# Kernel optimization log

Measured on AMD Instinct MI355X. Metric: run time of the kernel, lower is better.

The kernel has to match this reference:

```python
import jax, jax.numpy as jnp
import numpy as np

H, HD, C = 16, 64, 64            # num_heads, head_dim, mini_batch_size
BASE_LR = 1.0
EPS = 1e-6                        # ttt LN eps (ln_fwd / ln_fused_l2_bwd)


def _l2norm(x):
    return x / jnp.maximum(jnp.linalg.norm(x, axis=-1, keepdims=True), 1e-12)


def _ln_fwd(x, g, b):
    mu = x.mean(-1, keepdims=True)
    var = x.var(-1, keepdims=True)
    return g * ((x - mu) * jax.lax.rsqrt(var + EPS)) + b


def _ln_l2_bwd(x, tgt, g, b):
    # gradient of ||LN(x)*g+b - tgt||^2 / 2 wrt x
    D = x.shape[-1]
    mu = x.mean(-1, keepdims=True)
    var = x.var(-1, keepdims=True)
    std = jnp.sqrt(var + EPS)
    xh = (x - mu) / std
    gout = (g * xh + b) - tgt
    gxh = gout * g
    return (D * gxh - gxh.sum(-1, keepdims=True) - xh * (gxh * xh).sum(-1, keepdims=True)) / (D * std)


def setup_inputs() -> dict:
    key = jax.random.key(0)
    ks = jax.random.split(key, 12)
    B, L, D = 4, 8192, 1024
    std = 0.02
    return {
        'hidden_states': jax.random.normal(ks[0], (B, L, D), jnp.float32),
        'wq_w': jax.random.normal(ks[1], (D, D), jnp.float32) * std,
        'wq_b': jnp.zeros((D,), jnp.float32),
        'wk_w': jax.random.normal(ks[2], (D, D), jnp.float32) * std,
        'wk_b': jnp.zeros((D,), jnp.float32),
        'wv_w': jax.random.normal(ks[3], (D, D), jnp.float32) * std,
        'wv_b': jnp.zeros((D,), jnp.float32),
        'wo_w': jax.random.normal(ks[4], (D, D), jnp.float32) * std,
        'wo_b': jnp.zeros((D,), jnp.float32),
        'ttt_norm_weight': jnp.ones((H, HD), jnp.float32),
        'ttt_norm_bias': jnp.zeros((H, HD), jnp.float32),
        'ttt_lr_weight': jax.random.normal(ks[5], (H, 1, D), jnp.float32) * std,
        'ttt_lr_bias': jnp.zeros((H, 1), jnp.float32),
        'W1': jax.random.normal(ks[6], (H, HD, HD), jnp.float32) * std,
        'b1': jnp.zeros((H, 1, HD), jnp.float32),
        'post_norm_w': jnp.ones((D,), jnp.float32),
        'post_norm_b': jnp.zeros((D,), jnp.float32),
    }


def _forward(hidden_states, wq_w, wq_b, wk_w, wk_b, wv_w, wv_b, wo_w, wo_b,
             ttt_norm_weight, ttt_norm_bias, ttt_lr_weight, ttt_lr_bias,
             W1, b1, post_norm_w, post_norm_b):
    B, L, D = hidden_states.shape
    NC = L // C
    XQ = (hidden_states @ wq_w.T + wq_b).reshape(B, L, H, HD)
    XK = (hidden_states @ wk_w.T + wk_b).reshape(B, L, H, HD)
    XV = (hidden_states @ wv_w.T + wv_b).reshape(B, L, H, HD)
    XQ = _l2norm(XQ)
    XK = _l2norm(XK)
    # ln_reconstruction_target (uses sample std, ddof=1, eps=1e-5 on std)
    d = XV - XK
    mu = d.mean(-1, keepdims=True)
    sd = d.std(-1, keepdims=True, ddof=1)
    XV = ttt_norm_weight[None, None] * ((d - mu) / (sd + 1e-5)) + ttt_norm_bias[None, None] + XK
    # reshape to mini-batches: [B,H,NC,C,HD]
    Xmb = hidden_states.reshape(B, NC, C, D)
    to_mb = lambda t: t.transpose(0, 2, 1, 3).reshape(B, H, NC, C, HD)
    XQ, XK, XV = to_mb(XQ), to_mb(XK), to_mb(XV)
    # eta: sigmoid lr gate per token, row-broadcast over mini-batch
    ttt_lr = jax.nn.sigmoid(jnp.einsum('bnkc,hdc->bhnkd', Xmb, ttt_lr_weight)
                            + ttt_lr_bias.reshape(1, H, 1, 1, 1))     # [B,H,NC,C,1]
    eta = jnp.swapaxes(ttt_lr, -1, -2) * (BASE_LR / HD / C)           # [B,H,NC,1,C]
    mask = jnp.tril(jnp.ones((C, C), hidden_states.dtype))
    g = ttt_norm_weight[None, :, None, :]
    bta = ttt_norm_bias[None, :, None, :]
    W0 = jnp.broadcast_to(W1[None], (B, H, HD, HD))
    b0 = jnp.broadcast_to(b1[None], (B, H, 1, HD))

    def step(carry, xs):
        W, bvec = carry
        xq, xk, xv, eta_row = xs                      # eta_row: [B,H,1,C]
        Z1 = xk @ W + bvec                            # [B,H,C,HD]
        grad = _ln_l2_bwd(Z1, xv - xk, g, bta)        # [B,H,C,HD]
        Attn = mask * jnp.einsum('bhid,bhjd->bhij', xq, xk)   # [B,H,C,C]
        eta_full = jnp.broadcast_to(eta_row, Attn.shape)      # [B,H,C,C]
        b1_bar = bvec - (mask * eta_full) @ grad              # [B,H,C,HD]
        Z1_bar = xq @ W - (eta_full * Attn) @ grad + b1_bar
        last_eta = eta_full[..., -1, :, None]                 # [B,H,C,1]
        W_new = W - jnp.einsum('bhcd,bhce->bhde', last_eta * xk, grad)
        b_new = bvec - (last_eta * grad).sum(-2, keepdims=True)
        out = xq + _ln_fwd(Z1_bar, g, bta)
        return (W_new, b_new), out

    xs = (jnp.moveaxis(XQ, 2, 0), jnp.moveaxis(XK, 2, 0),
          jnp.moveaxis(XV, 2, 0), jnp.moveaxis(eta, 2, 0))
    _, outs = jax.lax.scan(step, (W0, b0), xs)        # outs: [NC,B,H,C,HD]
    y = jnp.moveaxis(outs, 0, 2).reshape(B, H, L, HD).transpose(0, 2, 1, 3).reshape(B, L, D)
    # post LayerNorm (eps=1e-6) + output projection
    mu2 = y.mean(-1, keepdims=True)
    var2 = y.var(-1, keepdims=True)
    y = post_norm_w * ((y - mu2) * jax.lax.rsqrt(var2 + 1e-6)) + post_norm_b
    return y @ wo_w.T + wo_b


def reference(hidden_states, wq_w, wq_b, wk_w, wk_b, wv_w, wv_b, wo_w, wo_b,
              ttt_norm_weight, ttt_norm_bias, ttt_lr_weight, ttt_lr_bias,
              W1, b1, post_norm_w, post_norm_b):
    return _forward(hidden_states, wq_w, wq_b, wk_w, wk_b, wv_w, wv_b, wo_w, wo_b,
                    ttt_norm_weight, ttt_norm_bias, ttt_lr_weight, ttt_lr_bias,
                    W1, b1, post_norm_w, post_norm_b)
```

## Files before the change

kernel.cpp:

```cpp
#include <hip/hip_runtime.h>


typedef __attribute__((ext_vector_type(8))) short short8;
typedef __attribute__((ext_vector_type(4))) float f32x4;
typedef __attribute__((ext_vector_type(4))) unsigned short us4;

__device__ __forceinline__ float bf2f(unsigned short s) {
  union { unsigned int u; float f; } c;
  c.u = ((unsigned int)s) << 16;
  return c.f;
}
__device__ __forceinline__ unsigned short f2bf(float f) {
  union { float f; unsigned int u; } c;
  c.f = f;
  unsigned int u = c.u;
  return (unsigned short)((u + 0x7FFFu + ((u >> 16) & 1u)) >> 16);
}

__device__ __forceinline__ void gload_lds16(const void* g, void* l) {
  __builtin_amdgcn_global_load_lds(
      (const __attribute__((address_space(1))) unsigned int*)g,
      (__attribute__((address_space(3))) unsigned int*)l, 16, 0, 0);
}

__device__ __forceinline__ float dpp16_sum(float x) {
  int v = __float_as_int(x);
  x += __int_as_float(__builtin_amdgcn_update_dpp(v, v, 0xB1, 0xF, 0xF, true));
  v = __float_as_int(x);
  x += __int_as_float(__builtin_amdgcn_update_dpp(v, v, 0x4E, 0xF, 0xF, true));
  v = __float_as_int(x);
  x += __int_as_float(__builtin_amdgcn_update_dpp(v, v, 0x141, 0xF, 0xF, true));
  v = __float_as_int(x);
  x += __int_as_float(__builtin_amdgcn_update_dpp(v, v, 0x140, 0xF, 0xF, true));
  return x;
}

__device__ __forceinline__ void barrier_fast() {
  __builtin_amdgcn_sched_barrier(0);
  asm volatile("s_waitcnt lgkmcnt(0)" ::: "memory");
  __builtin_amdgcn_s_barrier();
  asm volatile("" ::: "memory");
  __builtin_amdgcn_sched_barrier(0);
}
__device__ __forceinline__ void bar_nowait() {
  __builtin_amdgcn_sched_barrier(0);
  asm volatile("" ::: "memory");
  __builtin_amdgcn_s_barrier();
  asm volatile("" ::: "memory");
  __builtin_amdgcn_sched_barrier(0);
}

__global__ __launch_bounds__(256) void cvt_f32_bf16(
    const float* __restrict__ in, unsigned short* __restrict__ out, long n) {
  long i = ((long)blockIdx.x * 256 + threadIdx.x) * 4;
  if (i + 3 < n) {
    float4 v = *(const float4*)&in[i];
    us4 o = { f2bf(v.x), f2bf(v.y), f2bf(v.z), f2bf(v.w) };
    *(us4*)&out[i] = o;
  }
}

__global__ __launch_bounds__(256) void build_wcat(
    const float* __restrict__ wq, const float* __restrict__ wk,
    const float* __restrict__ wv, const float* __restrict__ lrw,
    const float* __restrict__ wqb, const float* __restrict__ wkb,
    const float* __restrict__ wvb, const float* __restrict__ lrb,
    unsigned short* __restrict__ Wcat, float* __restrict__ biasc) {
  int i = blockIdx.x * 256 + threadIdx.x;
  int row = i >> 10, col = i & 1023;
  int h = row >> 8, o = row & 255;
  float v;
  if (o < 64)        v = wq[(h * 64 + o) * 1024 + col];
  else if (o < 128)  v = wk[(h * 64 + o - 64) * 1024 + col];
  else if (o < 192)  v = wv[(h * 64 + o - 128) * 1024 + col];
  else if (o == 192) v = lrw[h * 1024 + col];
  else               v = 0.f;
  Wcat[i] = f2bf(v);
  if (i < 4096) {
    int hh = i >> 8, oo = i & 255;
    float bv;
    if (oo < 64)        bv = wqb[hh * 64 + oo];
    else if (oo < 128)  bv = wkb[hh * 64 + oo - 64];
    else if (oo < 192)  bv = wvb[hh * 64 + oo - 128];
    else if (oo == 192) bv = lrb[hh];
    else                bv = 0.f;
    biasc[i] = bv;
  }
}


__global__ __launch_bounds__(512, 1) void gemm256_qkv(
    const unsigned short* __restrict__ A, const unsigned short* __restrict__ B,
    const float* __restrict__ bias, const float* __restrict__ tnw,
    const float* __restrict__ tnb, unsigned short* __restrict__ XQn,
    unsigned short* __restrict__ XKn, unsigned short* __restrict__ TGT,
    float* __restrict__ eta, long M, long K) {
  __shared__ __align__(16) unsigned short g_lds[49152];
  char* ldsc = (char*)g_lds;
  const int tid = threadIdx.x, lane = tid & 63, wid = tid >> 6;
  const int wm = wid >> 2, wn = wid & 3;
  const int l15 = lane & 15, lg = lane >> 4;
  const int NTILN = 16;

  unsigned nwg = gridDim.x, bid = blockIdx.x;
  unsigned cpx = nwg >> 3;
  unsigned swz = (bid & 7) * cpx + (bid >> 3);
  unsigned nidx = swz % (unsigned)NTILN, midx = swz / (unsigned)NTILN;
  const long m0 = (long)midx * 256, n0 = (long)nidx * 256;
  const long ldab = K * 2;

  const int srow = wid * 16 + (lane >> 2);
  const int scol = ((lane & 3) * 16) ^ (((lane >> 3) & 3) << 4);
  const int sdst = wid * 1024;
  const char* Ab = (const char*)A;
  const char* Bb = (const char*)B;

  const int acol = (lg * 16) ^ (((l15 >> 1) & 3) << 4);
  const int aro = (wm * 128 + l15) * 64 + acol;
  const int bro = 16384 + (wn * 64 + l15) * 64 + acol;

#define STG_A(tt, h, bb)                                                      \
  gload_lds16(Ab + (size_t)(m0 + (h) * 128 + srow) * ldab + (size_t)(tt) * 64 \
                  + scol,                                                     \
              ldsc + (bb) * 32768 + (h) * 8192 + sdst)
#define STG_B(tt, h, bb)                                                      \
  gload_lds16(Bb + (size_t)(n0 + (h) * 128 + srow) * ldab + (size_t)(tt) * 64 \
                  + scol,                                                     \
              ldsc + (bb) * 32768 + 16384 + (h) * 8192 + sdst)

  f32x4 acc[8][4];
#pragma unroll
  for (int m = 0; m < 8; ++m)
#pragma unroll
    for (int n = 0; n < 4; ++n) acc[m][n] = (f32x4){0.f, 0.f, 0.f, 0.f};

  const int NT = (int)(K >> 5);

  STG_A(0, 0, 0); STG_A(0, 1, 0); STG_B(0, 0, 0); STG_B(0, 1, 0);
  STG_A(1, 0, 1); STG_A(1, 1, 1); STG_B(1, 0, 1); STG_B(1, 1, 1);
  asm volatile("s_waitcnt vmcnt(4)" ::: "memory");
  bar_nowait();

  int buf = 0, sb = 2;
#pragma unroll 1
  for (int t = 0; t < NT; ++t) {
    if (t + 2 < NT) {
      STG_A(t + 2, 0, sb); STG_A(t + 2, 1, sb);
      STG_B(t + 2, 0, sb); STG_B(t + 2, 1, sb);
    }
    const char* ab = ldsc + buf * 32768 + aro;
    const char* bb2 = ldsc + buf * 32768 + bro;
    short8 av[8], bv[4];
#pragma unroll
    for (int i = 0; i < 8; ++i) av[i] = *(const short8*)(ab + i * 1024);
#pragma unroll
    for (int nf = 0; nf < 4; ++nf) bv[nf] = *(const short8*)(bb2 + nf * 1024);
    __builtin_amdgcn_s_setprio(1);
#pragma unroll
    for (int i = 0; i < 8; ++i)
#pragma unroll
      for (int nf = 0; nf < 4; ++nf)
        acc[i][nf] = __builtin_amdgcn_mfma_f32_16x16x32_bf16(av[i], bv[nf],
                                                             acc[i][nf], 0, 0, 0);
    __builtin_amdgcn_s_setprio(0);
    asm volatile("s_waitcnt vmcnt(4)" ::: "memory");
    bar_nowait();
    buf = (buf == 2) ? 0 : buf + 1;
    sb = (sb == 2) ? 0 : sb + 1;
  }
#undef STG_A
#undef STG_B

  const int h = (int)nidx;
  float bcol[4], twv[4], tbv[4];
#pragma unroll
  for (int nf = 0; nf < 4; ++nf) {
    bcol[nf] = bias[n0 + wn * 64 + nf * 16 + l15];
    twv[nf] = tnw[h * 64 + nf * 16 + l15];
    tbv[nf] = tnb[h * 64 + nf * 16 + l15];
  }
  __syncthreads();
  unsigned short* kn_s = g_lds;

  if (wn == 0) {
#pragma unroll
    for (int mf = 0; mf < 8; ++mf)
#pragma unroll
      for (int j = 0; j < 4; ++j) {
        float v[4], s2 = 0.f;
#pragma unroll
        for (int nf = 0; nf < 4; ++nf) {
          v[nf] = acc[mf][nf][j] + bcol[nf];
          s2 += v[nf] * v[nf];
        }
        s2 = dpp16_sum(s2);
        float rn = 1.f / fmaxf(sqrtf(s2), 1e-12f);
        size_t tt = (size_t)(m0 + wm * 128 + mf * 16 + lg * 4 + j);
#pragma unroll
        for (int nf = 0; nf < 4; ++nf)
          XQn[tt * 1024 + h * 64 + nf * 16 + l15] = f2bf(v[nf] * rn);
      }
  } else if (wn == 1) {
#pragma unroll
    for (int mf = 0; mf < 8; ++mf)
#pragma unroll
      for (int j = 0; j < 4; ++j) {
        float v[4], s2 = 0.f;
#pragma unroll
        for (int nf = 0; nf < 4; ++nf) {
          v[nf] = acc[mf][nf][j] + bcol[nf];
          s2 += v[nf] * v[nf];
        }
        s2 = dpp16_sum(s2);
        float rn = 1.f / fmaxf(sqrtf(s2), 1e-12f);
        size_t tt = (size_t)(m0 + wm * 128 + mf * 16 + lg * 4 + j);
        int lr_ = wm * 128 + mf * 16 + lg * 4 + j;
#pragma unroll
        for (int nf = 0; nf < 4; ++nf) {
          unsigned short kb = f2bf(v[nf] * rn);
          XKn[tt * 1024 + h * 64 + nf * 16 + l15] = kb;
          kn_s[lr_ * 72 + nf * 16 + l15] = kb;
        }
      }
  }
  __syncthreads();
  if (wn == 2) {
#pragma unroll
    for (int mf = 0; mf < 8; ++mf)
#pragma unroll
      for (int j = 0; j < 4; ++j) {
        int lr_ = wm * 128 + mf * 16 + lg * 4 + j;
        float dv[4], s1 = 0.f, s2 = 0.f;
#pragma unroll
        for (int nf = 0; nf < 4; ++nf) {
          float kn = bf2f(kn_s[lr_ * 72 + nf * 16 + l15]);
          dv[nf] = acc[mf][nf][j] + bcol[nf] - kn;
          s1 += dv[nf];
          s2 += dv[nf] * dv[nf];
        }
        s1 = dpp16_sum(s1);
        s2 = dpp16_sum(s2);
        float mu = s1 * 0.015625f;
        float var1 = fmaxf(s2 - 64.f * mu * mu, 0.f) * (1.f / 63.f);
        float rs = 1.f / (sqrtf(var1) + 1e-5f);
        size_t tt = (size_t)(m0 + wm * 128 + mf * 16 + lg * 4 + j);
#pragma unroll
        for (int nf = 0; nf < 4; ++nf)
          TGT[tt * 1024 + h * 64 + nf * 16 + l15] =
              f2bf(twv[nf] * ((dv[nf] - mu) * rs) + tbv[nf]);
      }
  } else if (wn == 3 && l15 == 0) {
#pragma unroll
    for (int mf = 0; mf < 8; ++mf)
#pragma unroll
      for (int j = 0; j < 4; ++j) {
        size_t tt = (size_t)(m0 + wm * 128 + mf * 16 + lg * 4 + j);
        float lgt = acc[mf][0][j] + bcol[0];
        float sig = 1.f / (1.f + expf(-lgt));
        eta[((tt >> 13) * 16 + h) * 8192 + (tt & 8191)] = sig * (1.f / 4096.f);
      }
  }
}

template <int WRITE_BF16>
__global__ __launch_bounds__(512, 1) void gemm256(
    const unsigned short* __restrict__ A, const unsigned short* __restrict__ B,
    const float* __restrict__ bias, void* __restrict__ Cout,
    long M, long N, long K, int NTILN, long ldc) {
  __shared__ __align__(16) unsigned short g_lds[49152];
  char* ldsc = (char*)g_lds;
  const int tid = threadIdx.x, lane = tid & 63, wid = tid >> 6;
  const int wm = wid >> 2, wn = wid & 3;
  const int l15 = lane & 15, lg = lane >> 4;

  unsigned nwg = gridDim.x, bid = blockIdx.x;
  unsigned cpx = nwg >> 3;
  unsigned swz = (bid & 7) * cpx + (bid >> 3);
  unsigned nidx = swz % (unsigned)NTILN, midx = swz / (unsigned)NTILN;
  const long m0 = (long)midx * 256, n0 = (long)nidx * 256;
  const long ldab = K * 2;

  const int srow = wid * 16 + (lane >> 2);
  const int scol = ((lane & 3) * 16) ^ (((lane >> 3) & 3) << 4);
  const int sdst = wid * 1024;
  const char* Ab = (const char*)A;
  const char* Bb = (const char*)B;

  const int acol = (lg * 16) ^ (((l15 >> 1) & 3) << 4);
  const int aro = (wm * 128 + l15) * 64 + acol;
  const int bro = 16384 + (wn * 64 + l15) * 64 + acol;

#define STG_A(tt, h, bb)                                                      \
  gload_lds16(Ab + (size_t)(m0 + (h) * 128 + srow) * ldab + (size_t)(tt) * 64 \
                  + scol,                                                     \
              ldsc + (bb) * 32768 + (h) * 8192 + sdst)
#define STG_B(tt, h, bb)                                                      \
  gload_lds16(Bb + (size_t)(n0 + (h) * 128 + srow) * ldab + (size_t)(tt) * 64 \
                  + scol,                                                     \
              ldsc + (bb) * 32768 + 16384 + (h) * 8192 + sdst)

  f32x4 acc[8][4];
#pragma unroll
  for (int m = 0; m < 8; ++m)
#pragma unroll
    for (int n = 0; n < 4; ++n) acc[m][n] = (f32x4){0.f, 0.f, 0.f, 0.f};

  const int NT = (int)(K >> 5);

  STG_A(0, 0, 0); STG_A(0, 1, 0); STG_B(0, 0, 0); STG_B(0, 1, 0);
  STG_A(1, 0, 1); STG_A(1, 1, 1); STG_B(1, 0, 1); STG_B(1, 1, 1);
  asm volatile("s_waitcnt vmcnt(4)" ::: "memory");
  bar_nowait();

  int buf = 0, sb = 2;
#pragma unroll 1
  for (int t = 0; t < NT; ++t) {
    if (t + 2 < NT) {
      STG_A(t + 2, 0, sb); STG_A(t + 2, 1, sb);
      STG_B(t + 2, 0, sb); STG_B(t + 2, 1, sb);
    }
    const char* ab = ldsc + buf * 32768 + aro;
    const char* bb2 = ldsc + buf * 32768 + bro;
    short8 av[8], bv[4];
#pragma unroll
    for (int i = 0; i < 8; ++i) av[i] = *(const short8*)(ab + i * 1024);
#pragma unroll
    for (int nf = 0; nf < 4; ++nf) bv[nf] = *(const short8*)(bb2 + nf * 1024);
    __builtin_amdgcn_s_setprio(1);
#pragma unroll
    for (int i = 0; i < 8; ++i)
#pragma unroll
      for (int nf = 0; nf < 4; ++nf)
        acc[i][nf] = __builtin_amdgcn_mfma_f32_16x16x32_bf16(av[i], bv[nf],
                                                             acc[i][nf], 0, 0, 0);
    __builtin_amdgcn_s_setprio(0);
    asm volatile("s_waitcnt vmcnt(4)" ::: "memory");
    bar_nowait();
    buf = (buf == 2) ? 0 : buf + 1;
    sb = (sb == 2) ? 0 : sb + 1;
  }
#undef STG_A
#undef STG_B

#pragma unroll
  for (int mf = 0; mf < 8; ++mf) {
    long r0 = m0 + wm * 128 + mf * 16 + lg * 4;
#pragma unroll
    for (int nf = 0; nf < 4; ++nf) {
      long c = n0 + wn * 64 + nf * 16 + l15;
      float bvv = bias ? bias[c] : 0.f;
#pragma unroll
      for (int j = 0; j < 4; ++j) {
        float v = acc[mf][nf][j] + bvv;
        if (WRITE_BF16)
          ((unsigned short*)Cout)[(r0 + j) * ldc + c] = f2bf(v);
        else
          ((float*)Cout)[(r0 + j) * ldc + c] = v;
      }
    }
  }
}

__global__ __launch_bounds__(512, 1) void ttt_scan(
    const unsigned short* __restrict__ XQ, const unsigned short* __restrict__ XK,
    const unsigned short* __restrict__ TG, const float* __restrict__ eta_buf,
    const float* __restrict__ W1, const float* __restrict__ b1,
    const float* __restrict__ tnw, const float* __restrict__ tnb,
    float* __restrict__ y) {
  const int bh = blockIdx.x;
  const int b = bh >> 4, h = bh & 15;
  const int tid = threadIdx.x;
  const int lane = tid & 63, wid = tid >> 6;
  const bool isA = wid < 4;
  const int q = wid & 3;
  const int l15 = lane & 15, lg = lane >> 4;

  __shared__ __align__(16) unsigned short xq_s[2][64 * 72];
  __shared__ __align__(16) unsigned short tg_s[2][64 * 72];
  __shared__ __align__(16) unsigned short xk_s[2][64 * 72];
  __shared__ __align__(16) unsigned short gc_s[64 * 72];
  __shared__ __align__(16) unsigned short gradT[64 * 72];
  __shared__ __align__(16) unsigned short xkTe[64 * 72];
  __shared__ __align__(16) unsigned short WT_b[2][64 * 72];
  __shared__ float eta_s[2][64];
  __shared__ float bpart[4][64];

  const size_t tokb = (size_t)b * 8192;
  const int col0 = h * 64;
  const int rr_ = q * 16 + (lane >> 3);
  const int c8_ = (lane & 7) * 8;

  short8 pA0[2], pA1[2], pB0[2];
  float peta = 0.f;
  float bstv[4], gwv[4], gbv[4];
  f32x4 Wreg[4];

  if (isA) {
#pragma unroll
    for (int n = 0; n < 4; ++n) {
      int e = n * 16 + l15;
      bstv[n] = b1[h * 64 + e];
      gwv[n] = tnw[h * 64 + e];
      gbv[n] = tnb[h * 64 + e];
    }
#pragma unroll
    for (int j = 0; j < 2; ++j) {
      size_t g = (tokb + rr_ + j * 8) * 1024 + col0 + c8_;
      pA0[j] = *(const short8*)&XQ[g];
      pA1[j] = *(const short8*)&TG[g];
    }
#pragma unroll
    for (int j = 0; j < 2; ++j) {
      int rr = rr_ + j * 8;
      *(short8*)&xq_s[0][rr * 72 + c8_] = pA0[j];
      *(short8*)&tg_s[0][rr * 72 + c8_] = pA1[j];
    }
#pragma unroll
    for (int j = 0; j < 2; ++j) {
      size_t g = (tokb + 64 + rr_ + j * 8) * 1024 + col0 + c8_;
      pA0[j] = *(const short8*)&XQ[g];
      pA1[j] = *(const short8*)&TG[g];
    }
  } else {
#pragma unroll
    for (int j = 0; j < 2; ++j)
      pB0[j] = *(const short8*)&XK[(tokb + rr_ + j * 8) * 1024 + col0 + c8_];
#pragma unroll
    for (int j = 0; j < 2; ++j)
      *(short8*)&xk_s[0][(rr_ + j * 8) * 72 + c8_] = pB0[j];
#pragma unroll
    for (int j = 0; j < 2; ++j)
      pB0[j] = *(const short8*)&XK[(tokb + 64 + rr_ + j * 8) * 1024 + col0 + c8_];
#pragma unroll
    for (int n = 0; n < 4; ++n)
#pragma unroll
      for (int jj = 0; jj < 4; ++jj) {
        int d = q * 16 + lg * 4 + jj, e = n * 16 + l15;
        float w = W1[h * 4096 + d * 64 + e];
        Wreg[n][jj] = w;
        WT_b[0][e * 72 + d] = f2bf(w);
      }
    if (wid == 4) {
      eta_s[0][lane] = eta_buf[(size_t)bh * 8192 + lane];
      peta = eta_buf[(size_t)bh * 8192 + 64 + lane];
    }
  }
  __syncthreads();

  for (int nc = 0; nc < 128; ++nc) {
    const int p = nc & 1;
    const unsigned short* WTc = WT_b[p];
    unsigned short* WTn = WT_b[p ^ 1];

    if (isA) {
      if (nc) {
#pragma unroll
        for (int n = 0; n < 4; ++n) {
          int e = n * 16 + l15;
          bstv[n] -= bpart[0][e] + bpart[1][e] + bpart[2][e] + bpart[3][e];
        }
      }
      if (nc + 1 < 128) {
#pragma unroll
        for (int j = 0; j < 2; ++j) {
          int rr = rr_ + j * 8;
          *(short8*)&xq_s[p ^ 1][rr * 72 + c8_] = pA0[j];
          *(short8*)&tg_s[p ^ 1][rr * 72 + c8_] = pA1[j];
        }
      }
      if (nc + 2 < 128) {
#pragma unroll
        for (int j = 0; j < 2; ++j) {
          size_t g = (tokb + (nc + 2) * 64 + rr_ + j * 8) * 1024 + col0 + c8_;
          pA0[j] = *(const short8*)&XQ[g];
          pA1[j] = *(const short8*)&TG[g];
        }
      }
      f32x4 accZ[4];
#pragma unroll
      for (int n = 0; n < 4; ++n)
        accZ[n] = (f32x4){bstv[n], bstv[n], bstv[n], bstv[n]};
      __builtin_amdgcn_s_setprio(1);
#pragma unroll
      for (int kk = 0; kk < 2; ++kk) {
        const int ko = kk * 32 + lg * 8;
        short8 a_xk = *(const short8*)&xk_s[p][(q * 16 + l15) * 72 + ko];
#pragma unroll
        for (int n = 0; n < 4; ++n) {
          short8 b_w = *(const short8*)&WTc[(n * 16 + l15) * 72 + ko];
          accZ[n] = __builtin_amdgcn_mfma_f32_16x16x32_bf16(a_xk, b_w, accZ[n], 0, 0, 0);
        }
      }
      __builtin_amdgcn_s_setprio(0);
      float grv[4][4];
#pragma unroll
      for (int j = 0; j < 4; ++j) {
        const int r = q * 16 + lg * 4 + j;
        float z[4], s1 = 0.f, s2 = 0.f;
#pragma unroll
        for (int n = 0; n < 4; ++n) {
          z[n] = accZ[n][j];
          s1 += z[n];
          s2 += z[n] * z[n];
        }
        s1 = dpp16_sum(s1);
        s2 = dpp16_sum(s2);
        float mu = s1 * 0.015625f;
        float var = s2 * 0.015625f - mu * mu;
        float rstd = rsqrtf(var + 1e-6f);
        float xh[4], gx[4], s3 = 0.f, s4 = 0.f;
#pragma unroll
        for (int n = 0; n < 4; ++n) {
          xh[n] = (z[n] - mu) * rstd;
          float tg = bf2f(tg_s[p][r * 72 + n * 16 + l15]);
          float go = gwv[n] * xh[n] + gbv[n] - tg;
          gx[n] = go * gwv[n];
          s3 += gx[n];
          s4 += gx[n] * xh[n];
        }
        s3 = dpp16_sum(s3);
        s4 = dpp16_sum(s4);
#pragma unroll
        for (int n = 0; n < 4; ++n)
          grv[n][j] = (64.f * gx[n] - s3 - xh[n] * s4) * rstd * 0.015625f;
      }
#pragma unroll
      for (int n = 0; n < 4; ++n) {
        us4 pk = {f2bf(grv[n][0]), f2bf(grv[n][1]), f2bf(grv[n][2]),
                  f2bf(grv[n][3])};
        *(us4*)&gradT[(n * 16 + l15) * 72 + q * 16 + lg * 4] = pk;
      }
    } else {
      if (nc + 1 < 128) {
#pragma unroll
        for (int j = 0; j < 2; ++j)
          *(short8*)&xk_s[p ^ 1][(rr_ + j * 8) * 72 + c8_] = pB0[j];
        if (wid == 4) eta_s[p ^ 1][lane] = peta;
      }
      if (nc + 2 < 128) {
#pragma unroll
        for (int j = 0; j < 2; ++j)
          pB0[j] = *(const short8*)
              &XK[(tokb + (nc + 2) * 64 + rr_ + j * 8) * 1024 + col0 + c8_];
        if (wid == 4) peta = eta_buf[(size_t)bh * 8192 + (nc + 2) * 64 + lane];
      }
#pragma unroll
      for (int it = 0; it < 4; ++it) {
        int c0 = q * 16 + it * 4;
        us4 pk;
#pragma unroll
        for (int u = 0; u < 4; ++u)
          pk[u] = f2bf(-eta_s[p][c0 + u] * bf2f(xk_s[p][(c0 + u) * 72 + lane]));
        *(us4*)&xkTe[lane * 72 + c0] = pk;
      }
      f32x4 accA[4];
#pragma unroll
      for (int n = 0; n < 4; ++n) accA[n] = (f32x4){0.f, 0.f, 0.f, 0.f};
      __builtin_amdgcn_s_setprio(1);
#pragma unroll
      for (int kk = 0; kk < 2; ++kk) {
        const int ko = kk * 32 + lg * 8;
        short8 a_xq = *(const short8*)&xq_s[p][(q * 16 + l15) * 72 + ko];
#pragma unroll
        for (int n = 0; n < 4; ++n) {
          short8 b_k = *(const short8*)&xk_s[p][(n * 16 + l15) * 72 + ko];
          accA[n] = __builtin_amdgcn_mfma_f32_16x16x32_bf16(a_xq, b_k, accA[n], 0, 0, 0);
        }
      }
      __builtin_amdgcn_s_setprio(0);
#pragma unroll
      for (int j = 0; j < 4; ++j) {
        const int r = q * 16 + lg * 4 + j;
#pragma unroll
        for (int n = 0; n < 4; ++n) {
          int cj = n * 16 + l15;
          float v = (cj <= r) ? (-eta_s[p][cj] * (1.f + accA[n][j])) : 0.f;
          gc_s[r * 72 + cj] = f2bf(v);
        }
      }
    }
    barrier_fast();

    if (isA) {
      f32x4 accZb[4];
#pragma unroll
      for (int n = 0; n < 4; ++n)
        accZb[n] = (f32x4){bstv[n], bstv[n], bstv[n], bstv[n]};
      __builtin_amdgcn_s_setprio(1);
#pragma unroll
      for (int kk = 0; kk < 2; ++kk) {
        const int ko = kk * 32 + lg * 8;
        short8 a_xq = *(const short8*)&xq_s[p][(q * 16 + l15) * 72 + ko];
        short8 a_gc = *(const short8*)&gc_s[(q * 16 + l15) * 72 + ko];
#pragma unroll
        for (int n = 0; n < 4; ++n) {
          short8 b_w = *(const short8*)&WTc[(n * 16 + l15) * 72 + ko];
          short8 b_g = *(const short8*)&gradT[(n * 16 + l15) * 72 + ko];
          accZb[n] = __builtin_amdgcn_mfma_f32_16x16x32_bf16(a_xq, b_w, accZb[n], 0, 0, 0);
          accZb[n] = __builtin_amdgcn_mfma_f32_16x16x32_bf16(a_gc, b_g, accZb[n], 0, 0, 0);
        }
      }
      __builtin_amdgcn_s_setprio(0);
#pragma unroll
      for (int j = 0; j < 4; ++j) {
        const int r = q * 16 + lg * 4 + j;
        float z[4], s1 = 0.f, s2 = 0.f;
#pragma unroll
        for (int n = 0; n < 4; ++n) {
          z[n] = accZb[n][j];
          s1 += z[n];
          s2 += z[n] * z[n];
        }
        s1 = dpp16_sum(s1);
        s2 = dpp16_sum(s2);
        float mu = s1 * 0.015625f;
        float var = s2 * 0.015625f - mu * mu;
        float rstd = rsqrtf(var + 1e-6f);
        size_t gbase = (tokb + nc * 64 + r) * 1024 + col0;
#pragma unroll
        for (int n = 0; n < 4; ++n) {
          int e = n * 16 + l15;
          float ov = bf2f(xq_s[p][r * 72 + e]) + gwv[n] * ((z[n] - mu) * rstd) + gbv[n];
          y[gbase + e] = ov;
        }
      }
    } else {
      short8 a_ke[2], b_g[2][4];
#pragma unroll
      for (int kk = 0; kk < 2; ++kk) {
        const int ko = kk * 32 + lg * 8;
        a_ke[kk] = *(const short8*)&xkTe[(q * 16 + l15) * 72 + ko];
#pragma unroll
        for (int n = 0; n < 4; ++n)
          b_g[kk][n] = *(const short8*)&gradT[(n * 16 + l15) * 72 + ko];
      }
      f32x4 accW[4];
#pragma unroll
      for (int n = 0; n < 4; ++n) accW[n] = Wreg[n];
      __builtin_amdgcn_s_setprio(1);
#pragma unroll
      for (int kk = 0; kk < 2; ++kk)
#pragma unroll
        for (int n = 0; n < 4; ++n)
          accW[n] = __builtin_amdgcn_mfma_f32_16x16x32_bf16(a_ke[kk], b_g[kk][n],
                                                            accW[n], 0, 0, 0);
      __builtin_amdgcn_s_setprio(0);
#pragma unroll
      for (int n = 0; n < 4; ++n) {
        Wreg[n] = accW[n];
        us4 pk = {f2bf(accW[n][0]), f2bf(accW[n][1]), f2bf(accW[n][2]),
                  f2bf(accW[n][3])};
        *(us4*)&WTn[(n * 16 + l15) * 72 + q * 16 + lg * 4] = pk;
      }
      {
        float s = 0.f;
#pragma unroll
        for (int it = 0; it < 4; ++it) {
          us4 gv = *(const us4*)&gradT[lane * 72 + q * 16 + it * 4];
#pragma unroll
          for (int u = 0; u < 4; ++u)
            s += eta_s[p][q * 16 + it * 4 + u] * bf2f(gv[u]);
        }
        bpart[q][lane] = s;
      }
    }
    barrier_fast();
  }
}

__global__ __launch_bounds__(256) void postnorm(
    const float* __restrict__ yv, const float* __restrict__ pw,
    const float* __restrict__ pb, unsigned short* __restrict__ yn) {
  int t = blockIdx.x;
  int tid = threadIdx.x, lane = tid & 63, wid = tid >> 6;
  const float* row = yv + (size_t)t * 1024;
  float4 v = *(const float4*)&row[tid * 4];
  float s1 = v.x + v.y + v.z + v.w;
  float s2 = v.x * v.x + v.y * v.y + v.z * v.z + v.w * v.w;
#pragma unroll
  for (int o = 1; o < 64; o <<= 1) {
    s1 += __shfl_xor(s1, o);
    s2 += __shfl_xor(s2, o);
  }
  __shared__ float r1[4], r2[4];
  if (lane == 0) {
    r1[wid] = s1;
    r2[wid] = s2;
  }
  __syncthreads();
  s1 = r1[0] + r1[1] + r1[2] + r1[3];
  s2 = r2[0] + r2[1] + r2[2] + r2[3];
  float mu = s1 * (1.f / 1024.f);
  float var = s2 * (1.f / 1024.f) - mu * mu;
  float rstd = rsqrtf(var + 1e-6f);
  int c = tid * 4;
  us4 o4 = {f2bf(pw[c] * ((v.x - mu) * rstd) + pb[c]),
            f2bf(pw[c + 1] * ((v.y - mu) * rstd) + pb[c + 1]),
            f2bf(pw[c + 2] * ((v.z - mu) * rstd) + pb[c + 2]),
            f2bf(pw[c + 3] * ((v.w - mu) * rstd) + pb[c + 3])};
  *(us4*)&yn[(size_t)t * 1024 + c] = o4;
}

extern "C" void kernel_launch(void* const* d_in, const int* in_sizes, int n_in,
                              void* d_out, int out_size, void* d_ws,
                              size_t ws_size, hipStream_t stream) {
  const float* hs  = (const float*)d_in[0];
  const float* wqw = (const float*)d_in[1];
  const float* wqb = (const float*)d_in[2];
  const float* wkw = (const float*)d_in[3];
  const float* wkb = (const float*)d_in[4];
  const float* wvw = (const float*)d_in[5];
  const float* wvb = (const float*)d_in[6];
  const float* wow = (const float*)d_in[7];
  const float* wob = (const float*)d_in[8];
  const float* tnw = (const float*)d_in[9];
  const float* tnb = (const float*)d_in[10];
  const float* lrw = (const float*)d_in[11];
  const float* lrb = (const float*)d_in[12];
  const float* W1  = (const float*)d_in[13];
  const float* b1  = (const float*)d_in[14];
  const float* pnw = (const float*)d_in[15];
  const float* pnb = (const float*)d_in[16];

  const size_t OFF_XQ    = 0;
  const size_t OFF_XK    = 67108864;
  const size_t OFF_TGT   = 134217728;
  const size_t OFF_ETA   = 201326592;
  const size_t OFF_WOBF  = OFF_ETA + 2097152;
  const size_t OFF_HSBF  = OFF_WOBF + 2097152;
  const size_t OFF_WCAT  = OFF_HSBF + 67108864;
  const size_t OFF_BIASC = OFF_WCAT + 8388608;
  const size_t OFF_YV    = OFF_HSBF;
  const size_t NEEDED_A  = OFF_BIASC + 16384;
  const size_t NEEDED_B  = OFF_YV + 134217728;
  const size_t NEEDED    = NEEDED_A > NEEDED_B ? NEEDED_A : NEEDED_B;
  if (ws_size < NEEDED) return;

  char* ws = (char*)d_ws;
  unsigned short* XQn   = (unsigned short*)(ws + OFF_XQ);
  unsigned short* ynorm = (unsigned short*)(ws + OFF_XQ);
  unsigned short* XKn   = (unsigned short*)(ws + OFF_XK);
  unsigned short* TGT   = (unsigned short*)(ws + OFF_TGT);
  float* eta_buf        = (float*)(ws + OFF_ETA);
  unsigned short* wo_bf = (unsigned short*)(ws + OFF_WOBF);
  unsigned short* hs_bf = (unsigned short*)(ws + OFF_HSBF);
  unsigned short* Wcat  = (unsigned short*)(ws + OFF_WCAT);
  float* biasc          = (float*)(ws + OFF_BIASC);
  float* yv             = (float*)(ws + OFF_YV);

  cvt_f32_bf16<<<32768, 256, 0, stream>>>(hs, hs_bf, 33554432L);
  build_wcat<<<16384, 256, 0, stream>>>(wqw, wkw, wvw, lrw, wqb, wkb, wvb, lrb,
                                        Wcat, biasc);
  cvt_f32_bf16<<<1024, 256, 0, stream>>>(wow, wo_bf, 1048576L);
  gemm256_qkv<<<2048, 512, 0, stream>>>(hs_bf, Wcat, biasc, tnw, tnb,
                                        XQn, XKn, TGT, eta_buf, 32768L, 1024L);
  ttt_scan<<<64, 512, 0, stream>>>(XQn, XKn, TGT, eta_buf, W1, b1, tnw, tnb, yv);
  postnorm<<<32768, 256, 0, stream>>>(yv, pnw, pnb, ynorm);
  gemm256<0><<<512, 512, 0, stream>>>(ynorm, wo_bf, wob, d_out,
                                      32768L, 1024L, 1024L, 4, 1024L);
}
```

Baseline: 889.1 us.

## Deepen GEMM LDS pipeline to four stages and split MFMA phases

Both 256x256 GEMM kernels move from a triple-buffered LDS pipeline to four buffers, prefetching three K-tiles ahead. This grows shared memory to 128KB per block. Each iteration is split into two half-tile MFMA phases with interleaved LDS reads and global-to-LDS stage issues, plus explicit barriers and scheduling fences. The aim is to hide global load latency and lower register pressure (4 A fragments at a time instead of 8). The cost is more barriers per iteration and a larger LDS footprint.

```diff
diff --git a/kernel.cpp b/kernel.cpp
--- a/kernel.cpp
+++ b/kernel.cpp
@@ -88,6 +88,55 @@
   }
 }
 
+#define GEMM_MAIN_LOOP()                                                      \
+  const int NT = (int)(K >> 5);                                               \
+  _Pragma("unroll") for (int tt = 0; tt < 3; ++tt) {                          \
+    STG_A(tt, 0, tt); STG_A(tt, 1, tt);                                       \
+    STG_B(tt, 0, tt); STG_B(tt, 1, tt);                                       \
+  }                                                                           \
+  asm volatile("s_waitcnt vmcnt(8)" ::: "memory");                            \
+  bar_nowait();                                                               \
+  _Pragma("unroll 1") for (int t = 0; t < NT; ++t) {                          \
+    const int buf = t & 3, sb = (t + 3) & 3;                                  \
+    const bool doStage = (t + 3 < NT);                                        \
+    const char* ab = ldsc + buf * 32768 + aro;                                \
+    const char* bb2 = ldsc + buf * 32768 + bro;                               \
+    short8 av[4], bv[4];                                                      \
+    _Pragma("unroll") for (int i = 0; i < 4; ++i)                             \
+        av[i] = *(const short8*)(ab + i * 1024);                              \
+    _Pragma("unroll") for (int nf = 0; nf < 4; ++nf)                          \
+        bv[nf] = *(const short8*)(bb2 + nf * 1024);                           \
+    if (doStage) { STG_A(t + 3, 0, sb); STG_A(t + 3, 1, sb); }                \
+    bar_nowait();                                                             \
+    asm volatile("s_waitcnt lgkmcnt(0)" ::: "memory");                        \
+    __builtin_amdgcn_sched_barrier(0);                                        \
+    __builtin_amdgcn_s_setprio(1);                                            \
+    _Pragma("unroll") for (int i = 0; i < 4; ++i)                             \
+        _Pragma("unroll") for (int nf = 0; nf < 4; ++nf)                      \
+            acc[i][nf] = __builtin_amdgcn_mfma_f32_16x16x32_bf16(             \
+                av[i], bv[nf], acc[i][nf], 0, 0, 0);                          \
+    __builtin_amdgcn_s_setprio(0);                                            \
+    bar_nowait();                                                             \
+    _Pragma("unroll") for (int i = 0; i < 4; ++i)                             \
+        av[i] = *(const short8*)(ab + 4096 + i * 1024);                       \
+    if (doStage) { STG_B(t + 3, 0, sb); STG_B(t + 3, 1, sb); }                \
+    bar_nowait();                                                             \
+    asm volatile("s_waitcnt lgkmcnt(0)" ::: "memory");                        \
+    __builtin_amdgcn_sched_barrier(0);                                        \
+    __builtin_amdgcn_s_setprio(1);                                            \
+    _Pragma("unroll") for (int i = 0; i < 4; ++i)                             \
+        _Pragma("unroll") for (int nf = 0; nf < 4; ++nf)                      \
+            acc[4 + i][nf] = __builtin_amdgcn_mfma_f32_16x16x32_bf16(         \
+                av[i], bv[nf], acc[4 + i][nf], 0, 0, 0);                      \
+    __builtin_amdgcn_s_setprio(0);                                            \
+    if (t < NT - 3)                                                           \
+      asm volatile("s_waitcnt vmcnt(8)" ::: "memory");                        \
+    else if (t == NT - 3)                                                     \
+      asm volatile("s_waitcnt vmcnt(4)" ::: "memory");                        \
+    else                                                                      \
+      asm volatile("s_waitcnt vmcnt(0)" ::: "memory");                        \
+    bar_nowait();                                                             \
+  }
 
 __global__ __launch_bounds__(512, 1) void gemm256_qkv(
     const unsigned short* __restrict__ A, const unsigned short* __restrict__ B,
@@ -95,7 +144,7 @@
     const float* __restrict__ tnb, unsigned short* __restrict__ XQn,
     unsigned short* __restrict__ XKn, unsigned short* __restrict__ TGT,
     float* __restrict__ eta, long M, long K) {
-  __shared__ __align__(16) unsigned short g_lds[49152];
+  __shared__ __align__(16) unsigned short g_lds[65536];
   char* ldsc = (char*)g_lds;
   const int tid = threadIdx.x, lane = tid & 63, wid = tid >> 6;
   const int wm = wid >> 2, wn = wid & 3;
@@ -134,40 +183,7 @@
 #pragma unroll
     for (int n = 0; n < 4; ++n) acc[m][n] = (f32x4){0.f, 0.f, 0.f, 0.f};
 
-  const int NT = (int)(K >> 5);
-
-  STG_A(0, 0, 0); STG_A(0, 1, 0); STG_B(0, 0, 0); STG_B(0, 1, 0);
-  STG_A(1, 0, 1); STG_A(1, 1, 1); STG_B(1, 0, 1); STG_B(1, 1, 1);
-  asm volatile("s_waitcnt vmcnt(4)" ::: "memory");
-  bar_nowait();
-
-  int buf = 0, sb = 2;
-#pragma unroll 1
-  for (int t = 0; t < NT; ++t) {
-    if (t + 2 < NT) {
-      STG_A(t + 2, 0, sb); STG_A(t + 2, 1, sb);
-      STG_B(t + 2, 0, sb); STG_B(t + 2, 1, sb);
-    }
-    const char* ab = ldsc + buf * 32768 + aro;
-    const char* bb2 = ldsc + buf * 32768 + bro;
-    short8 av[8], bv[4];
-#pragma unroll
-    for (int i = 0; i < 8; ++i) av[i] = *(const short8*)(ab + i * 1024);
-#pragma unroll
-    for (int nf = 0; nf < 4; ++nf) bv[nf] = *(const short8*)(bb2 + nf * 1024);
-    __builtin_amdgcn_s_setprio(1);
-#pragma unroll
-    for (int i = 0; i < 8; ++i)
-#pragma unroll
-      for (int nf = 0; nf < 4; ++nf)
-        acc[i][nf] = __builtin_amdgcn_mfma_f32_16x16x32_bf16(av[i], bv[nf],
-                                                             acc[i][nf], 0, 0, 0);
-    __builtin_amdgcn_s_setprio(0);
-    asm volatile("s_waitcnt vmcnt(4)" ::: "memory");
-    bar_nowait();
-    buf = (buf == 2) ? 0 : buf + 1;
-    sb = (sb == 2) ? 0 : sb + 1;
-  }
+  GEMM_MAIN_LOOP()
 #undef STG_A
 #undef STG_B
 
@@ -267,7 +283,7 @@
     const unsigned short* __restrict__ A, const unsigned short* __restrict__ B,
     const float* __restrict__ bias, void* __restrict__ Cout,
     long M, long N, long K, int NTILN, long ldc) {
-  __shared__ __align__(16) unsigned short g_lds[49152];
+  __shared__ __align__(16) unsigned short g_lds[65536];
   char* ldsc = (char*)g_lds;
   const int tid = threadIdx.x, lane = tid & 63, wid = tid >> 6;
   const int wm = wid >> 2, wn = wid & 3;
@@ -305,40 +321,7 @@
 #pragma unroll
     for (int n = 0; n < 4; ++n) acc[m][n] = (f32x4){0.f, 0.f, 0.f, 0.f};
 
-  const int NT = (int)(K >> 5);
-
-  STG_A(0, 0, 0); STG_A(0, 1, 0); STG_B(0, 0, 0); STG_B(0, 1, 0);
-  STG_A(1, 0, 1); STG_A(1, 1, 1); STG_B(1, 0, 1); STG_B(1, 1, 1);
-  asm volatile("s_waitcnt vmcnt(4)" ::: "memory");
-  bar_nowait();
-
-  int buf = 0, sb = 2;
-#pragma unroll 1
-  for (int t = 0; t < NT; ++t) {
-    if (t + 2 < NT) {
-      STG_A(t + 2, 0, sb); STG_A(t + 2, 1, sb);
-      STG_B(t + 2, 0, sb); STG_B(t + 2, 1, sb);
-    }
-    const char* ab = ldsc + buf * 32768 + aro;
-    const char* bb2 = ldsc + buf * 32768 + bro;
-    short8 av[8], bv[4];
-#pragma unroll
-    for (int i = 0; i < 8; ++i) av[i] = *(const short8*)(ab + i * 1024);
-#pragma unroll
-    for (int nf = 0; nf < 4; ++nf) bv[nf] = *(const short8*)(bb2 + nf * 1024);
-    __builtin_amdgcn_s_setprio(1);
-#pragma unroll
-    for (int i = 0; i < 8; ++i)
-#pragma unroll
-      for (int nf = 0; nf < 4; ++nf)
-        acc[i][nf] = __builtin_amdgcn_mfma_f32_16x16x32_bf16(av[i], bv[nf],
-                                                             acc[i][nf], 0, 0, 0);
-    __builtin_amdgcn_s_setprio(0);
-    asm volatile("s_waitcnt vmcnt(4)" ::: "memory");
-    bar_nowait();
-    buf = (buf == 2) ? 0 : buf + 1;
-    sb = (sb == 2) ? 0 : sb + 1;
-  }
+  GEMM_MAIN_LOOP()
 #undef STG_A
 #undef STG_B
 
```

New measurement: 904.2 us. No clear change (+1.7%).
